# Performance work log

Measured on AMD Instinct MI355X. Metric: run time of the kernel, lower is better.

The kernel has to match this reference:

```python
import jax, jax.numpy as jnp
import numpy as np

DIM = 32  # fixed internal node dim
N_GRAPHS = 64


def setup_inputs() -> dict:
    key = jax.random.key(0)
    ks = jax.random.split(key, 16)
    N, E, F_N, F_E, H = 12500, 200000, 16, 8, 32
    inp = {
        "x": jax.random.normal(ks[0], (N, F_N), dtype=jnp.float32),
        "edge_index": jax.random.randint(ks[1], (2, E), 0, N, dtype=jnp.int64),
        "edge_attr": jax.random.normal(ks[2], (E, F_E), dtype=jnp.float32),
        "batch": jnp.sort(jax.random.randint(ks[3], (N,), 0, N_GRAPHS, dtype=jnp.int64)),
        "lin0_w": jax.random.normal(ks[4], (DIM, F_N), dtype=jnp.float32) * 0.1,
        "lin0_b": jax.random.normal(ks[5], (DIM,), dtype=jnp.float32) * 0.1,
        "nn_w": jax.random.normal(ks[6], (DIM * H, F_E), dtype=jnp.float32) * 0.1,
        "nn_b": jax.random.normal(ks[7], (DIM * H,), dtype=jnp.float32) * 0.1,
        "root_w": jax.random.normal(ks[8], (DIM, H), dtype=jnp.float32) * 0.1,
        "conv_b": jax.random.normal(ks[9], (H,), dtype=jnp.float32) * 0.1,
        "lin1_w": jax.random.normal(ks[10], (16, H), dtype=jnp.float32) * 0.1,
        "lin1_b": jax.random.normal(ks[11], (16,), dtype=jnp.float32) * 0.1,
        "lin2_w": jax.random.normal(ks[12], (1, 16), dtype=jnp.float32) * 0.1,
        "lin2_b": jax.random.normal(ks[13], (1,), dtype=jnp.float32) * 0.1,
    }
    return inp


def reference(x, edge_index, edge_attr, batch, lin0_w, lin0_b, nn_w, nn_b,
              root_w, conv_b, lin1_w, lin1_b, lin2_w, lin2_b):
    N = x.shape[0]
    H = conv_b.shape[0]
    # lin0 + relu -> node features [N, DIM]
    out = jax.nn.relu(x @ lin0_w.T + lin0_b)
    # NNConv: per-edge weight matrices from edge MLP (single Linear)
    src, dst = edge_index[0], edge_index[1]
    w_e = (edge_attr @ nn_w.T + nn_b).reshape(-1, DIM, H)  # [E, DIM, H]
    msg = jnp.einsum('ed,edh->eh', out[src], w_e)          # gather + per-edge matmul
    agg = jax.ops.segment_sum(msg, dst, num_segments=N)     # scatter-add
    h = jax.nn.relu(agg + out @ root_w + conv_b)             # root weight + bias
    # global add pool over graphs
    u = jax.ops.segment_sum(h, batch, num_segments=N_GRAPHS)  # [G, H]
    o = jax.nn.relu(u @ lin1_w.T + lin1_b)
    o = o @ lin2_w.T + lin2_b
    return o.reshape(-1)
```

## Files before the change

### kernel.cpp

```cpp
#include <hip/hip_runtime.h>

#define DIMN 32
#define HD   32
#define FN   16
#define FE   8
#define NG   64

__global__ __launch_bounds__(256) void k1_node_pre(
    const float* __restrict__ x, const float* __restrict__ lin0_w,
    const float* __restrict__ lin0_b, const float* __restrict__ nn_w,
    const float* __restrict__ nn_b,
    float* __restrict__ outn, float* __restrict__ G, float* __restrict__ bmsg,
    int N, int nodes_per_block)
{
    __shared__ float s_nnw[DIMN * HD * FE];
    __shared__ float s_nnb[DIMN * HD];
    __shared__ float s_l0w[DIMN * FN];
    __shared__ float s_l0b[DIMN];
    __shared__ float s_out[DIMN];

    const int tid = threadIdx.x;
    for (int i = tid; i < DIMN * HD * FE; i += 256) s_nnw[i] = nn_w[i];
    for (int i = tid; i < DIMN * HD; i += 256)      s_nnb[i] = nn_b[i];
    for (int i = tid; i < DIMN * FN; i += 256)      s_l0w[i] = lin0_w[i];
    if (tid < DIMN) s_l0b[tid] = lin0_b[tid];
    __syncthreads();

    const int n0 = blockIdx.x * nodes_per_block;
    const int n1 = min(n0 + nodes_per_block, N);
    for (int n = n0; n < n1; ++n) {
        if (tid < DIMN) {
            float s = s_l0b[tid];
            const float* xr = x + (size_t)n * FN;
            #pragma unroll
            for (int j = 0; j < FN; ++j) s = fmaf(xr[j], s_l0w[tid * FN + j], s);
            s = fmaxf(s, 0.f);
            s_out[tid] = s;
            outn[(size_t)n * DIMN + tid] = s;
        }
        __syncthreads();

        float g = 0.f;
        #pragma unroll 8
        for (int d = 0; d < DIMN; ++d)
            g = fmaf(s_out[d], s_nnw[d * 256 + tid], g);
        G[(size_t)n * 256 + tid] = g;

        if (tid < HD) {
            float b = 0.f;
            #pragma unroll 8
            for (int d = 0; d < DIMN; ++d)
                b = fmaf(s_out[d], s_nnb[d * HD + tid], b);
            bmsg[(size_t)n * HD + tid] = b;
        }
        __syncthreads();
    }
}

__global__ __launch_bounds__(256) void k2_edge(
    const int* __restrict__ ei, const float* __restrict__ ea,
    const float* __restrict__ G, const float* __restrict__ bmsg,
    float* __restrict__ agg, int E)
{
    const int t = blockIdx.x * 256 + threadIdx.x;
    const int e = t >> 5;
    const int h = t & 31;
    if (e >= E) return;

    const int src = ei[e];
    const int dst = ei[E + e];

    const float* gp = G + (size_t)src * 256 + h * 8;
    const float4 ga = *(const float4*)(gp);
    const float4 gb = *(const float4*)(gp + 4);
    const float4 e0 = *(const float4*)(ea + (size_t)e * 8);
    const float4 e1 = *(const float4*)(ea + (size_t)e * 8 + 4);

    float acc = bmsg[(size_t)src * HD + h];
    acc = fmaf(e0.x, ga.x, acc);
    acc = fmaf(e0.y, ga.y, acc);
    acc = fmaf(e0.z, ga.z, acc);
    acc = fmaf(e0.w, ga.w, acc);
    acc = fmaf(e1.x, gb.x, acc);
    acc = fmaf(e1.y, gb.y, acc);
    acc = fmaf(e1.z, gb.z, acc);
    acc = fmaf(e1.w, gb.w, acc);

    atomicAdd(agg + (size_t)dst * HD + h, acc);
}

__global__ __launch_bounds__(256) void k3_node_upd(
    const float* __restrict__ agg, const float* __restrict__ outn,
    const float* __restrict__ root_w, const float* __restrict__ conv_b,
    const int* __restrict__ batch, float* __restrict__ u, int N)
{
    __shared__ float s_rw[DIMN * HD];
    __shared__ float s_cb[HD];
    const int tid = threadIdx.x;
    for (int i = tid; i < DIMN * HD; i += 256) s_rw[i] = root_w[i];
    if (tid < HD) s_cb[tid] = conv_b[tid];
    __syncthreads();

    const int t = blockIdx.x * 256 + tid;
    const int n = t >> 5;
    const int h = t & 31;
    if (n >= N) return;

    float v = agg[(size_t)n * HD + h] + s_cb[h];
    const float* orow = outn + (size_t)n * DIMN;
    #pragma unroll 8
    for (int k = 0; k < DIMN; ++k)
        v = fmaf(orow[k], s_rw[k * HD + h], v);
    v = fmaxf(v, 0.f);

    atomicAdd(u + (size_t)batch[n] * HD + h, v);
}

__global__ __launch_bounds__(64) void k4_head(
    const float* __restrict__ u, const float* __restrict__ lin1_w,
    const float* __restrict__ lin1_b, const float* __restrict__ lin2_w,
    const float* __restrict__ lin2_b, float* __restrict__ outp)
{
    const int g = threadIdx.x;
    if (g >= NG) return;

    float ur[HD];
    #pragma unroll
    for (int hh = 0; hh < HD; ++hh) ur[hh] = u[(size_t)g * HD + hh];

    float acc = lin2_b[0];
    #pragma unroll
    for (int i = 0; i < 16; ++i) {
        float o = lin1_b[i];
        #pragma unroll
        for (int hh = 0; hh < HD; ++hh)
            o = fmaf(ur[hh], lin1_w[i * HD + hh], o);
        o = fmaxf(o, 0.f);
        acc = fmaf(o, lin2_w[i], acc);
    }
    outp[g] = acc;
}

extern "C" void kernel_launch(void* const* d_in, const int* in_sizes, int n_in,
                              void* d_out, int out_size, void* d_ws, size_t ws_size,
                              hipStream_t stream)
{
    const float* x      = (const float*)d_in[0];
    const int*   ei     = (const int*)  d_in[1];
    const float* ea     = (const float*)d_in[2];
    const int*   batch  = (const int*)  d_in[3];
    const float* lin0_w = (const float*)d_in[4];
    const float* lin0_b = (const float*)d_in[5];
    const float* nn_w   = (const float*)d_in[6];
    const float* nn_b   = (const float*)d_in[7];
    const float* root_w = (const float*)d_in[8];
    const float* conv_b = (const float*)d_in[9];
    const float* lin1_w = (const float*)d_in[10];
    const float* lin1_b = (const float*)d_in[11];
    const float* lin2_w = (const float*)d_in[12];
    const float* lin2_b = (const float*)d_in[13];

    const int N = in_sizes[0] / FN;
    const int E = in_sizes[2] / FE;

    float* ws   = (float*)d_ws;
    float* outn = ws;
    float* G    = outn + (size_t)N * DIMN;
    float* bmsg = G    + (size_t)N * 256;
    float* agg  = bmsg + (size_t)N * DIMN;
    float* u    = agg  + (size_t)N * DIMN;

    hipMemsetAsync(agg, 0, (size_t)N * DIMN * sizeof(float), stream);
    hipMemsetAsync(u,   0, (size_t)NG * HD * sizeof(float), stream);

    const int npb = 16;
    const int nb1 = (N + npb - 1) / npb;
    k1_node_pre<<<nb1, 256, 0, stream>>>(x, lin0_w, lin0_b, nn_w, nn_b,
                                         outn, G, bmsg, N, npb);

    const int nb2 = (E * 32 + 255) / 256;
    k2_edge<<<nb2, 256, 0, stream>>>(ei, ea, G, bmsg, agg, E);

    const int nb3 = (N * 32 + 255) / 256;
    k3_node_upd<<<nb3, 256, 0, stream>>>(agg, outn, root_w, conv_b, batch, u, N);

    k4_head<<<1, 64, 0, stream>>>(u, lin1_w, lin1_b, lin2_w, lin2_b, (float*)d_out);
}
```

Measured before the change: 173.5 us.

## Fuse buffer zeroing into node kernel, batch per-node sync, pre-reduce pool atomics

The two memset calls are removed, and zeroing of agg and u now happens inside the first node kernel. That kernel also computes lin0 for all 16 of its nodes at once instead of one node per synchronized iteration, which drops the per-node barriers. The node-update kernel gives each warp 8 consecutive nodes and accumulates in registers per graph id, so it issues far fewer atomics on the pooled output. This relies on batch being sorted to get the atomic reduction, and it relies on the u zeroing in k1 finishing before k3 runs, which stream ordering guarantees.

```diff
diff --git a/kernel.cpp b/kernel.cpp
--- a/kernel.cpp
+++ b/kernel.cpp
@@ -5,55 +5,77 @@
 #define FN   16
 #define FE   8
 #define NG   64
+#define NPB1 16
+#define NPB3 64
 
 __global__ __launch_bounds__(256) void k1_node_pre(
     const float* __restrict__ x, const float* __restrict__ lin0_w,
     const float* __restrict__ lin0_b, const float* __restrict__ nn_w,
     const float* __restrict__ nn_b,
     float* __restrict__ outn, float* __restrict__ G, float* __restrict__ bmsg,
-    int N, int nodes_per_block)
+    float* __restrict__ agg, float* __restrict__ u, int N)
 {
     __shared__ float s_nnw[DIMN * HD * FE];
     __shared__ float s_nnb[DIMN * HD];
     __shared__ float s_l0w[DIMN * FN];
     __shared__ float s_l0b[DIMN];
-    __shared__ float s_out[DIMN];
+    __shared__ float s_out[NPB1 * DIMN];
 
     const int tid = threadIdx.x;
     for (int i = tid; i < DIMN * HD * FE; i += 256) s_nnw[i] = nn_w[i];
     for (int i = tid; i < DIMN * HD; i += 256)      s_nnb[i] = nn_b[i];
     for (int i = tid; i < DIMN * FN; i += 256)      s_l0w[i] = lin0_w[i];
     if (tid < DIMN) s_l0b[tid] = lin0_b[tid];
+
+    const int n0 = blockIdx.x * NPB1;
+
+    {
+        const int a0 = n0 * HD;
+        const int a1 = min((n0 + NPB1) * HD, N * HD);
+        for (int i = a0 + tid; i < a1; i += 256) agg[i] = 0.f;
+        if (blockIdx.x < (NG * HD) / 256) u[blockIdx.x * 256 + tid] = 0.f;
+    }
     __syncthreads();
 
-    const int n0 = blockIdx.x * nodes_per_block;
-    const int n1 = min(n0 + nodes_per_block, N);
-    for (int n = n0; n < n1; ++n) {
-        if (tid < DIMN) {
-            float s = s_l0b[tid];
+    #pragma unroll
+    for (int pass = 0; pass < 2; ++pass) {
+        const int nl = pass * 8 + (tid >> 5);
+        const int d  = tid & 31;
+        const int n  = n0 + nl;
+        if (n < N) {
+            float s = s_l0b[d];
             const float* xr = x + (size_t)n * FN;
             #pragma unroll
-            for (int j = 0; j < FN; ++j) s = fmaf(xr[j], s_l0w[tid * FN + j], s);
+            for (int j = 0; j < FN; ++j) s = fmaf(xr[j], s_l0w[d * FN + j], s);
             s = fmaxf(s, 0.f);
-            s_out[tid] = s;
-            outn[(size_t)n * DIMN + tid] = s;
+            s_out[nl * DIMN + d] = s;
+            outn[(size_t)n * DIMN + d] = s;
         }
-        __syncthreads();
-
+    }
+    __syncthreads();
+
+    for (int nl = 0; nl < NPB1; ++nl) {
+        const int n = n0 + nl;
+        if (n >= N) break;
         float g = 0.f;
         #pragma unroll 8
         for (int d = 0; d < DIMN; ++d)
-            g = fmaf(s_out[d], s_nnw[d * 256 + tid], g);
+            g = fmaf(s_out[nl * DIMN + d], s_nnw[d * 256 + tid], g);
         G[(size_t)n * 256 + tid] = g;
-
-        if (tid < HD) {
+    }
+
+    #pragma unroll
+    for (int pass = 0; pass < 2; ++pass) {
+        const int nl = pass * 8 + (tid >> 5);
+        const int h  = tid & 31;
+        const int n  = n0 + nl;
+        if (n < N) {
             float b = 0.f;
             #pragma unroll 8
             for (int d = 0; d < DIMN; ++d)
-                b = fmaf(s_out[d], s_nnb[d * HD + tid], b);
-            bmsg[(size_t)n * HD + tid] = b;
+                b = fmaf(s_out[nl * DIMN + d], s_nnb[d * HD + h], b);
+            bmsg[(size_t)n * HD + h] = b;
         }
-        __syncthreads();
     }
 }
 
@@ -101,19 +123,34 @@
     if (tid < HD) s_cb[tid] = conv_b[tid];
     __syncthreads();
 
-    const int t = blockIdx.x * 256 + tid;
-    const int n = t >> 5;
-    const int h = t & 31;
-    if (n >= N) return;
-
-    float v = agg[(size_t)n * HD + h] + s_cb[h];
-    const float* orow = outn + (size_t)n * DIMN;
-    #pragma unroll 8
-    for (int k = 0; k < DIMN; ++k)
-        v = fmaf(orow[k], s_rw[k * HD + h], v);
-    v = fmaxf(v, 0.f);
-
-    atomicAdd(u + (size_t)batch[n] * HD + h, v);
+    const int sg   = tid >> 5;
+    const int h    = tid & 31;
+    const int base = blockIdx.x * NPB3 + sg * (NPB3 / 8);
+
+    float acc  = 0.f;
+    int  g_cur = -1;
+    #pragma unroll
+    for (int i = 0; i < NPB3 / 8; ++i) {
+        const int n = base + i;
+        if (n >= N) break;
+
+        float v = agg[(size_t)n * HD + h] + s_cb[h];
+        const float* orow = outn + (size_t)n * DIMN;
+        #pragma unroll 8
+        for (int k = 0; k < DIMN; ++k)
+            v = fmaf(orow[k], s_rw[k * HD + h], v);
+        v = fmaxf(v, 0.f);
+
+        const int g = (int)batch[n];
+        if (g != g_cur) {
+            if (g_cur >= 0) atomicAdd(u + (size_t)g_cur * HD + h, acc);
+            g_cur = g;
+            acc = v;
+        } else {
+            acc += v;
+        }
+    }
+    if (g_cur >= 0) atomicAdd(u + (size_t)g_cur * HD + h, acc);
 }
 
 __global__ __launch_bounds__(64) void k4_head(
@@ -170,18 +207,14 @@
     float* agg  = bmsg + (size_t)N * DIMN;
     float* u    = agg  + (size_t)N * DIMN;
 
-    hipMemsetAsync(agg, 0, (size_t)N * DIMN * sizeof(float), stream);
-    hipMemsetAsync(u,   0, (size_t)NG * HD * sizeof(float), stream);
-
-    const int npb = 16;
-    const int nb1 = (N + npb - 1) / npb;
+    const int nb1 = (N + NPB1 - 1) / NPB1;
     k1_node_pre<<<nb1, 256, 0, stream>>>(x, lin0_w, lin0_b, nn_w, nn_b,
-                                         outn, G, bmsg, N, npb);
+                                         outn, G, bmsg, agg, u, N);
 
     const int nb2 = (E * 32 + 255) / 256;
     k2_edge<<<nb2, 256, 0, stream>>>(ei, ea, G, bmsg, agg, E);
 
-    const int nb3 = (N * 32 + 255) / 256;
+    const int nb3 = (N + NPB3 - 1) / NPB3;
     k3_node_upd<<<nb3, 256, 0, stream>>>(agg, outn, root_w, conv_b, batch, u, N);
 
     k4_head<<<1, 64, 0, stream>>>(u, lin1_w, lin1_b, lin2_w, lin2_b, (float*)d_out);
```

Measured after the change: 157.9 us. 9.0% less time.
